# Kernel tuning notes

Measured on AMD Instinct MI355X. Metric: run time of the kernel, lower is better.

The kernel has to match this reference:

```python
import jax, jax.numpy as jnp
import numpy as np

N_NODES = 50000
N_EDGES = 800000
D_IN = 128
D_HID = 128
N_CLS = 40


def setup_inputs() -> dict:
    key = jax.random.key(0)
    ks = jax.random.split(key, 9)
    x = jax.random.normal(ks[0], (N_NODES, D_IN), dtype=jnp.float32)
    edge_index = jax.random.randint(ks[1], (2, N_EDGES), 0, N_NODES, dtype=jnp.int64)
    def lin(k, fan_in, fan_out):
        bound = 1.0 / np.sqrt(fan_in)
        return jax.random.uniform(k, (fan_in, fan_out), jnp.float32, -bound, bound)
    params = {
        'w1_l': lin(ks[2], D_IN, D_HID), 'w1_r': lin(ks[3], D_IN, D_HID),
        'b1': jnp.zeros((D_HID,), jnp.float32),
        'w2_l': lin(ks[4], D_HID, D_HID), 'w2_r': lin(ks[5], D_HID, D_HID),
        'b2': jnp.zeros((D_HID,), jnp.float32),
        'w3_l': lin(ks[6], D_HID, N_CLS), 'w3_r': lin(ks[7], D_HID, N_CLS),
        'b3': jnp.zeros((N_CLS,), jnp.float32),
    }
    return {'x': x, 'edge_index': edge_index, **params}


def _sage_layer(x, src, dst, w_l, w_r, b):
    # mean-aggregate messages from src -> dst, then lin_l(agg) + lin_r(x) + b, relu
    msgs = x[src]                                             # [E, d] gather
    agg = jax.ops.segment_sum(msgs, dst, num_segments=x.shape[0])  # [N, d]
    deg = jax.ops.segment_sum(jnp.ones((src.shape[0],), x.dtype), dst,
                              num_segments=x.shape[0])        # [N]
    agg = agg / jnp.maximum(deg, 1.0)[:, None]
    out = agg @ w_l + x @ w_r + b
    return jax.nn.relu(out)  # dropout p=0.0 -> identity


def reference(x, edge_index, w1_l, w1_r, b1, w2_l, w2_r, b2, w3_l, w3_r, b3):
    src, dst = edge_index[0], edge_index[1]
    h = _sage_layer(x, src, dst, w1_l, w1_r, b1)
    h = _sage_layer(h, src, dst, w2_l, w2_r, b2)
    h = _sage_layer(h, src, dst, w3_l, w3_r, b3)
    return h
```

## Files before the change

kernel.cpp:

```cpp
#include <hip/hip_runtime.h>
#include <hip/hip_bf16.h>

#define NN 50000
#define NE 800000
#define DD 128
#define NCLS 40
#define NBK ((NN + 255) >> 8)
#define EPB 1024
#define PB ((NE + EPB - 1) / EPB)
#define CVB ((NN * DD / 4) / 256)
#define WB 384
#define SEMAX 5120

typedef _Float16 f16x8 __attribute__((ext_vector_type(8)));
typedef _Float16 f16x4 __attribute__((ext_vector_type(4)));
typedef float f32x4 __attribute__((ext_vector_type(4)));

__device__ __forceinline__ unsigned int pack2h(_Float16 a, _Float16 b) {
    union { _Float16 h[2]; unsigned int u; } c;
    c.h[0] = a; c.h[1] = b;
    return c.u;
}
__device__ __forceinline__ void unpack2h(unsigned int p, float& a, float& b) {
    union { unsigned int u; _Float16 h[2]; } c;
    c.u = p;
    a = (float)c.h[0]; b = (float)c.h[1];
}

__global__ void k_front(const int* __restrict__ ei, int* __restrict__ cellcnt,
                        int* __restrict__ celloff, unsigned int* __restrict__ pairs,
                        const float* __restrict__ x, unsigned short* __restrict__ xh,
                        const float* __restrict__ w1l, const float* __restrict__ w1r,
                        const float* __restrict__ w2l, const float* __restrict__ w2r,
                        const float* __restrict__ w3l, const float* __restrict__ w3r,
                        unsigned short* __restrict__ bt1h,
                        unsigned short* __restrict__ bt2h,
                        unsigned short* __restrict__ bt3h) {
    if (blockIdx.x >= PB + CVB) {
        int idx = blockIdx.x - (PB + CVB);
        int w = idx >> 1, half = idx & 1;
        int ks = w & 7, tmp = w >> 3;
        int nt = tmp & 7, layer = tmp >> 3;
        const int NT = (layer == 2) ? 3 : 8;
        const int NC = (layer == 2) ? NCLS : DD;
        if (nt >= NT) return;
        const float* wl = (layer == 0) ? w1l : (layer == 1) ? w2l : w3l;
        const float* wr = (layer == 0) ? w1r : (layer == 1) ? w2r : w3r;
        unsigned short* bh = (layer == 0) ? bt1h : (layer == 1) ? bt2h : bt3h;
        int t = threadIdx.x;
        int j = t & 7, lane = (t >> 3) + half * 32;
        int row = nt * 16 + (lane & 15);
        int k = ks * 32 + (lane >> 4) * 8 + j;
        float v = 0.f;
        if (row < NC)
            v = (k < 128) ? wl[(size_t)k * NC + row] : wr[(size_t)(k - 128) * NC + row];
        union { _Float16 f; unsigned short u; } ch;
        ch.f = (_Float16)v;
        bh[((size_t)(ks * NT + nt) * 64 + lane) * 8 + j] = ch.u;
        return;
    }
    if (blockIdx.x >= PB) {
        int i = (blockIdx.x - PB) * 256 + threadIdx.x;
        float4 v = ((const float4*)x)[i];
        f16x4 h;
        h[0] = (_Float16)v.x; h[1] = (_Float16)v.y;
        h[2] = (_Float16)v.z; h[3] = (_Float16)v.w;
        *(f16x4*)(xh + (size_t)i * 4) = h;
        return;
    }
    __shared__ int hist[NBK];
    __shared__ int s[256];
    __shared__ unsigned int sE[EPB];
    __shared__ int nz;
    const int t = threadIdx.x, blk = blockIdx.x;
    const int e0 = blk * EPB;
    if (t == 0) nz = 0;
    for (int i = t; i < NBK; i += 256) hist[i] = 0;
    __syncthreads();
    int any = 0;
    for (int i = t; i < EPB; i += 256)
        if (ei[2 * e0 + 2 * i + 1] != 0) any = 1;
    if (any) atomicOr(&nz, 1);
    __syncthreads();
    const int is64 = (nz == 0);
    unsigned int v[EPB / 256];
    int eb[EPB / 256], er[EPB / 256];
#pragma unroll
    for (int j = 0; j < EPB / 256; ++j) {
        int e = e0 + j * 256 + t;
        if (e < NE) {
            int sv, d;
            if (is64) { sv = ei[2 * e]; d = ei[2 * (NE + e)]; }
            else      { sv = ei[e];     d = ei[NE + e]; }
            v[j] = ((unsigned)sv << 16) | (unsigned)d;
            eb[j] = d >> 8;
            er[j] = atomicAdd(&hist[eb[j]], 1);
        } else {
            eb[j] = -1;
        }
    }
    __syncthreads();
    int hv = (t < NBK) ? hist[t] : 0;
    s[t] = hv;
    __syncthreads();
#pragma unroll
    for (int off = 1; off < 256; off <<= 1) {
        int u = (t >= off) ? s[t - off] : 0;
        __syncthreads();
        s[t] += u;
        __syncthreads();
    }
#pragma unroll
    for (int j = 0; j < EPB / 256; ++j)
        if (eb[j] >= 0) sE[s[eb[j]] - hist[eb[j]] + er[j]] = v[j];
    __syncthreads();
    ((uint4*)(pairs + (size_t)blk * EPB))[t] = ((const uint4*)sE)[t];
    for (int i = t; i < NBK; i += 256) {
        cellcnt[(size_t)i * PB + blk] = hist[i];
        celloff[(size_t)i * PB + blk] = s[i] - hist[i];
    }
}

__global__ void k_scan_ba(const int* __restrict__ cellcnt, int* __restrict__ bsum) {
    __shared__ int red[256];
    int b = blockIdx.x, t = threadIdx.x;
    int acc = 0;
    for (int i = t; i < PB; i += 256) acc += cellcnt[(size_t)b * PB + i];
    red[t] = acc;
    __syncthreads();
#pragma unroll
    for (int off = 128; off > 0; off >>= 1) {
        if (t < off) red[t] += red[t + off];
        __syncthreads();
    }
    if (t == 0) bsum[b] = red[0];
}

__global__ void k_fill2(const unsigned int* __restrict__ pairs,
                        const int* __restrict__ cellcnt,
                        const int* __restrict__ celloff,
                        const int* __restrict__ bsum,
                        int* __restrict__ row_ptr, int* __restrict__ srcs) {
    __shared__ unsigned int sE[SEMAX];
    __shared__ int hist[256];
    __shared__ int cur[256];
    __shared__ int sb[256];
    __shared__ int scnt;
    const int b = blockIdx.x, t = threadIdx.x;
    if (t < 256) {
        int v = (t < NBK) ? bsum[t] : 0;
        sb[t] = v;
    }
    if (t == 0) scnt = 0;
    if (t < 256) hist[t] = 0;
    __syncthreads();
#pragma unroll
    for (int off = 1; off < 256; off <<= 1) {
        int u = (t >= off && t < 256) ? sb[t - off] : 0;
        __syncthreads();
        if (t < 256) sb[t] += u;
        __syncthreads();
    }
    const int bbase = (b == 0) ? 0 : sb[b - 1];
    if (b == NBK - 1 && t == 0) row_ptr[NN] = sb[NBK - 1];
    for (int blk = t; blk < PB; blk += 512) {
        int cnt = cellcnt[(size_t)b * PB + blk];
        if (cnt) {
            int off = celloff[(size_t)b * PB + blk];
            int base = atomicAdd(&scnt, cnt);
            if (base + cnt <= SEMAX) {
                const unsigned int* pp = pairs + (size_t)blk * EPB + off;
                for (int j = 0; j < cnt; ++j) {
                    unsigned int v = pp[j];
                    sE[base + j] = v;
                    atomicAdd(&hist[v & 255u], 1);
                }
            }
        }
    }
    __syncthreads();
    int h = (t < 256) ? hist[t] : 0;
    if (t < 256) cur[t] = h;
    __syncthreads();
#pragma unroll
    for (int off = 1; off < 256; off <<= 1) {
        int u = (t >= off && t < 256) ? cur[t - off] : 0;
        __syncthreads();
        if (t < 256) cur[t] += u;
        __syncthreads();
    }
    if (t < 256) {
        int node = (b << 8) + t;
        int base = bbase + cur[t] - h;
        if (node < NN) row_ptr[node] = base;
        cur[t] = base;
    }
    __syncthreads();
    int total = min(scnt, SEMAX);
    for (int i = t; i < total; i += 512) {
        unsigned int v = sE[i];
        int pos = atomicAdd(&cur[v & 255u], 1);
        srcs[pos] = (int)(v >> 16);
    }
}

__global__ __launch_bounds__(256, 8)
void k_agg(const unsigned int* __restrict__ inh, const int* __restrict__ row_ptr,
           const int* __restrict__ srcs, unsigned int* __restrict__ oh) {
    int node = blockIdx.x * 4 + (threadIdx.x >> 6);
    if (node >= NN) return;
    int lane = threadIdx.x & 63;
    int b = row_ptr[node], e = row_ptr[node + 1];
    float a0 = 0.f, a1 = 0.f;
    int i = b;
    for (; i + 16 <= e; i += 16) {
        unsigned int p[16];
#pragma unroll
        for (int j = 0; j < 16; ++j)
            p[j] = inh[(size_t)srcs[i + j] * 64 + lane];
#pragma unroll
        for (int j = 0; j < 16; ++j) {
            float u0, u1;
            unpack2h(p[j], u0, u1);
            a0 += u0; a1 += u1;
        }
    }
    int rem = e - i;
    if (rem > 0) {
        int ce = e - 1;
        unsigned int p[16];
#pragma unroll
        for (int j = 0; j < 16; ++j) {
            int idx = i + j;
            if (idx > ce) idx = ce;
            p[j] = inh[(size_t)srcs[idx] * 64 + lane];
        }
#pragma unroll
        for (int j = 0; j < 16; ++j) {
            float u0, u1;
            unpack2h(p[j], u0, u1);
            if (j < rem) { a0 += u0; a1 += u1; }
        }
    }
    int deg = e - b;
    float inv = 1.0f / (float)(deg > 0 ? deg : 1);
    oh[(size_t)node * 64 + lane] = pack2h((_Float16)(a0 * inv), (_Float16)(a1 * inv));
}

template <int NT, int KPS, bool PACKOUT>
__launch_bounds__(256, 4)
__global__ void k_mfma(const unsigned short* __restrict__ A1h,
                       const unsigned short* __restrict__ A2h,
                       const unsigned short* __restrict__ Bthf,
                       const float* __restrict__ bias, float* __restrict__ outf,
                       unsigned short* __restrict__ outh, const int NC) {
    constexpr int STAGE_ELEMS = KPS * NT * 64 * 8;
    constexpr int STAGE_U4 = STAGE_ELEMS / 8;
    __shared__ unsigned short sBh[STAGE_ELEMS];

    const int tid = threadIdx.x;
    const int wave = tid >> 6, lane = tid & 63;
    const int quad = lane >> 4, mr = lane & 15;
    const int m0 = blockIdx.x * 64 + wave * 16;
    const int row = m0 + mr;
    const bool rok = row < NN;

    f32x4 acc[NT] = {};
    const f16x8 zero = {};

    auto aload = [&](int ks) -> f16x8 {
        const int ko = ((ks * 32) & 127) + quad * 8;
        const unsigned short* base = (ks < 4) ? A1h : A2h;
        return rok ? *(const f16x8*)(base + (size_t)row * 128 + ko) : zero;
    };

    f16x8 cah = aload(0), pah;

#pragma unroll
    for (int s = 0; s < 8 / KPS; ++s) {
        const uint4* gh = (const uint4*)(Bthf + (size_t)s * STAGE_ELEMS);
        uint4* lh = (uint4*)sBh;
        if (s) __syncthreads();
        for (int i = tid; i < STAGE_U4; i += 256) lh[i] = gh[i];
        __syncthreads();

#pragma unroll
        for (int kl = 0; kl < KPS; ++kl) {
            const int ks = s * KPS + kl;
            if (ks < 7) pah = aload(ks + 1);
#pragma unroll
            for (int n = 0; n < NT; ++n) {
                const int fo = ((kl * NT + n) * 64 + lane) * 8;
                f16x8 bh = *(const f16x8*)(sBh + fo);
                acc[n] = __builtin_amdgcn_mfma_f32_16x16x32_f16(cah, bh, acc[n], 0, 0, 0);
            }
            cah = pah;
        }
    }

#pragma unroll
    for (int n = 0; n < NT; ++n) {
        int col = n * 16 + mr;
        float bv = (col < NC) ? bias[col] : 0.f;
#pragma unroll
        for (int r = 0; r < 4; ++r) {
            int orow = m0 + quad * 4 + r;
            if (orow < NN && col < NC) {
                float v = acc[n][r] + bv;
                v = v > 0.f ? v : 0.f;
                if (PACKOUT) {
                    union { _Float16 f; unsigned short u; } ch;
                    ch.f = (_Float16)v;
                    outh[(size_t)orow * 128 + col] = ch.u;
                } else {
                    outf[(size_t)orow * NC + col] = v;
                }
            }
        }
    }
}

__global__ __launch_bounds__(256, 4)
void k_gemm3(const unsigned short* __restrict__ Ah,
             const unsigned short* __restrict__ Bthf,
             const float* __restrict__ bias,
             unsigned short* __restrict__ zh, float* __restrict__ yf) {
    __shared__ unsigned short sBh[8 * 3 * 64 * 8];
    const int tid = threadIdx.x;
    const int wave = tid >> 6, lane = tid & 63;
    const int quad = lane >> 4, mr = lane & 15;
    const int m0 = blockIdx.x * 64 + wave * 16;
    const int row = m0 + mr;
    const bool rok = row < NN;

    const uint4* gh = (const uint4*)Bthf;
    uint4* lh = (uint4*)sBh;
    for (int i = tid; i < (8 * 3 * 64 * 8) / 8; i += 256) lh[i] = gh[i];

    const f16x8 zero = {};
    f16x8 a[4];
#pragma unroll
    for (int j = 0; j < 4; ++j)
        a[j] = rok ? *(const f16x8*)(Ah + (size_t)row * 128 + j * 32 + quad * 8)
                   : zero;
    __syncthreads();

    f32x4 accl[3] = {}, accr[3] = {};
#pragma unroll
    for (int ks = 0; ks < 4; ++ks) {
#pragma unroll
        for (int n = 0; n < 3; ++n) {
            f16x8 bl = *(const f16x8*)(sBh + ((ks * 3 + n) * 64 + lane) * 8);
            accl[n] = __builtin_amdgcn_mfma_f32_16x16x32_f16(a[ks], bl, accl[n], 0, 0, 0);
            f16x8 br = *(const f16x8*)(sBh + (((ks + 4) * 3 + n) * 64 + lane) * 8);
            accr[n] = __builtin_amdgcn_mfma_f32_16x16x32_f16(a[ks], br, accr[n], 0, 0, 0);
        }
    }

#pragma unroll
    for (int n = 0; n < 3; ++n) {
        int col = n * 16 + mr;
        float bv = (col < NCLS) ? bias[col] : 0.f;
#pragma unroll
        for (int r = 0; r < 4; ++r) {
            int orow = m0 + quad * 4 + r;
            if (orow < NN) {
                union { _Float16 f; unsigned short u; } ch;
                ch.f = (_Float16)accl[n][r];
                zh[(size_t)orow * 64 + col] = ch.u;
                if (col < NCLS) yf[(size_t)orow * 40 + col] = accr[n][r] + bv;
            }
        }
    }
}

__global__ __launch_bounds__(256, 8)
void k_agg3(const unsigned int* __restrict__ zu,
            const int* __restrict__ row_ptr,
            const int* __restrict__ srcs,
            const float* __restrict__ yf, float* __restrict__ out) {
    const int tid = threadIdx.x;
    const int wave = tid >> 6, lane = tid & 63;
    const int half = lane >> 5, hl = lane & 31;
    const int node = blockIdx.x * 8 + wave * 2 + half;
    int b = row_ptr[node], e = row_ptr[node + 1];
    int deg = e - b;
    int od = __shfl_xor(deg, 32);
    int md = max(deg, od);
    int ce = (e > b) ? (e - 1) : b;
    float a0 = 0.f, a1 = 0.f;
    for (int base = 0; base < md; base += 16) {
        unsigned int p[16];
#pragma unroll
        for (int j = 0; j < 16; ++j) {
            int idx = b + base + j;
            if (idx > ce) idx = ce;
            p[j] = zu[(size_t)srcs[idx] * 32 + hl];
        }
#pragma unroll
        for (int j = 0; j < 16; ++j) {
            float u0, u1;
            unpack2h(p[j], u0, u1);
            if (base + j < deg) { a0 += u0; a1 += u1; }
        }
    }
    float inv = 1.0f / (float)(deg > 0 ? deg : 1);
    if (hl < 20) {
        float2 yv = ((const float2*)yf)[(size_t)node * 20 + hl];
        float2 o;
        o.x = fmaxf(a0 * inv + yv.x, 0.f);
        o.y = fmaxf(a1 * inv + yv.y, 0.f);
        ((float2*)out)[(size_t)node * 20 + hl] = o;
    }
}

extern "C" void kernel_launch(void* const* d_in, const int* in_sizes, int n_in,
                              void* d_out, int out_size, void* d_ws, size_t ws_size,
                              hipStream_t stream) {
    const float* x    = (const float*)d_in[0];
    const int*   ei   = (const int*)d_in[1];
    const float* w1_l = (const float*)d_in[2];
    const float* w1_r = (const float*)d_in[3];
    const float* b1   = (const float*)d_in[4];
    const float* w2_l = (const float*)d_in[5];
    const float* w2_r = (const float*)d_in[6];
    const float* b2   = (const float*)d_in[7];
    const float* w3_l = (const float*)d_in[8];
    const float* w3_r = (const float*)d_in[9];
    const float* b3   = (const float*)d_in[10];
    float* out = (float*)d_out;

    char* w = (char*)d_ws;
    size_t off = 0;
    auto alloc = [&](size_t bytes) -> void* {
        void* p = w + off;
        off += (bytes + 255) / 256 * 256;
        return p;
    };
    int* row_ptr = (int*)alloc((size_t)(NN + 1) * 4);
    int* srcs    = (int*)alloc((size_t)NE * 4);
    int* cellcnt = (int*)alloc((size_t)NBK * PB * 4);
    int* celloff = (int*)alloc((size_t)NBK * PB * 4);
    int* bsum    = (int*)alloc((size_t)NBK * 4);
    unsigned int* pairs = (unsigned int*)alloc((size_t)PB * EPB * 4);
    unsigned short* xh   = (unsigned short*)alloc((size_t)NN * DD * 2);
    unsigned short* aggh = (unsigned short*)alloc((size_t)NN * DD * 2);
    unsigned short* h1h  = (unsigned short*)alloc((size_t)NN * DD * 2);
    unsigned short* zh   = (unsigned short*)alloc((size_t)NN * 64 * 2);
    float*          yf   = (float*)alloc((size_t)NN * 40 * 4);
    unsigned short* bt1h = (unsigned short*)alloc((size_t)8 * 8 * 64 * 8 * 2);
    unsigned short* bt2h = (unsigned short*)alloc((size_t)8 * 8 * 64 * 8 * 2);
    unsigned short* bt3h = (unsigned short*)alloc((size_t)8 * 3 * 64 * 8 * 2);
    unsigned short* h2h = xh;
    (void)ws_size;

    k_front<<<PB + CVB + WB, 256, 0, stream>>>(ei, cellcnt, celloff, pairs, x, xh,
                                               w1_l, w1_r, w2_l, w2_r, w3_l, w3_r,
                                               bt1h, bt2h, bt3h);
    k_scan_ba<<<NBK, 256, 0, stream>>>(cellcnt, bsum);
    k_fill2<<<NBK, 512, 0, stream>>>(pairs, cellcnt, celloff, bsum, row_ptr, srcs);

    const int gmb = (NN + 63) / 64;
    const int gab = (NN + 3) / 4;
    k_agg<<<gab, 256, 0, stream>>>((const unsigned int*)xh, row_ptr, srcs,
                                   (unsigned int*)aggh);
    k_mfma<8, 4, true><<<gmb, 256, 0, stream>>>(aggh, xh, bt1h, b1,
                                                nullptr, h1h, DD);
    k_agg<<<gab, 256, 0, stream>>>((const unsigned int*)h1h, row_ptr, srcs,
                                   (unsigned int*)aggh);
    k_mfma<8, 4, true><<<gmb, 256, 0, stream>>>(aggh, h1h, bt2h, b2,
                                                nullptr, h2h, DD);
    k_gemm3<<<gmb, 256, 0, stream>>>(h2h, bt3h, b3, zh, yf);
    k_agg3<<<NN / 8, 256, 0, stream>>>((const unsigned int*)zh, row_ptr, srcs,
                                       yf, out);
}
```

Baseline: 232.7 us.

## Split feature tables into column planes and use 16-bit source indices

Node feature tables are stored as four 32-column fp16 planes (each N x 64 bytes) instead of row-major 256-byte rows. The aggregation kernel now processes one plane per block, with blocks grouped by node pair and interleaved across planes, so each plane's gather working set is smaller and more likely to stay in cache. Source indices are narrowed to unsigned short to halve index traffic. The GEMM loads and stores are rewritten for the plane layout. Each gathered row segment is now only 64 bytes, which is short for coalescing. The 16-bit index is only valid because the packed value from the fill step holds the source in its upper 16 bits, and 50000 fits in that range.

```diff
diff --git a/kernel.cpp b/kernel.cpp
--- a/kernel.cpp
+++ b/kernel.cpp
@@ -26,6 +26,7 @@
     c.u = p;
     a = (float)c.h[0]; b = (float)c.h[1];
 }
+
 
 __global__ void k_front(const int* __restrict__ ei, int* __restrict__ cellcnt,
                         int* __restrict__ celloff, unsigned int* __restrict__ pairs,
@@ -65,7 +66,11 @@
         f16x4 h;
         h[0] = (_Float16)v.x; h[1] = (_Float16)v.y;
         h[2] = (_Float16)v.z; h[3] = (_Float16)v.w;
-        *(f16x4*)(xh + (size_t)i * 4) = h;
+        int row = i >> 5;
+        int f = i & 31;
+        int plane = f >> 3;
+        int pc = (f & 7) * 4;
+        *(f16x4*)(xh + ((size_t)plane * NN + row) * 32 + pc) = h;
         return;
     }
     __shared__ int hist[NBK];
@@ -140,7 +145,7 @@
                         const int* __restrict__ cellcnt,
                         const int* __restrict__ celloff,
                         const int* __restrict__ bsum,
-                        int* __restrict__ row_ptr, int* __restrict__ srcs) {
+                        int* __restrict__ row_ptr, unsigned short* __restrict__ srcs) {
     __shared__ unsigned int sE[SEMAX];
     __shared__ int hist[256];
     __shared__ int cur[256];
@@ -200,51 +205,48 @@
     for (int i = t; i < total; i += 512) {
         unsigned int v = sE[i];
         int pos = atomicAdd(&cur[v & 255u], 1);
-        srcs[pos] = (int)(v >> 16);
+        srcs[pos] = (unsigned short)(v >> 16);
     }
 }
 
 __global__ __launch_bounds__(256, 8)
-void k_agg(const unsigned int* __restrict__ inh, const int* __restrict__ row_ptr,
-           const int* __restrict__ srcs, unsigned int* __restrict__ oh) {
-    int node = blockIdx.x * 4 + (threadIdx.x >> 6);
-    if (node >= NN) return;
-    int lane = threadIdx.x & 63;
-    int b = row_ptr[node], e = row_ptr[node + 1];
+void k_agg8(const unsigned int* __restrict__ inq, const int* __restrict__ row_ptr,
+            const unsigned short* __restrict__ srcs, unsigned int* __restrict__ oq) {
+    const int tid = threadIdx.x;
+    const int quarter = (blockIdx.x & 7) >> 1;
+    const int parity  = blockIdx.x & 1;
+    const int node = ((blockIdx.x >> 3) * 2 + parity) * 16 + (tid >> 4);
+    const int pc = tid & 15;
+    const unsigned int* tab = inq + (size_t)quarter * NN * 16;
+    const int vn = node < NN ? node : NN - 1;
+    int b = row_ptr[vn], e = row_ptr[vn + 1];
+    int deg = (node < NN) ? (e - b) : 0;
+    int m = deg;
+    m = max(m, __shfl_xor(m, 16));
+    m = max(m, __shfl_xor(m, 32));
     float a0 = 0.f, a1 = 0.f;
-    int i = b;
-    for (; i + 16 <= e; i += 16) {
+    for (int base = 0; base < m; base += 16) {
         unsigned int p[16];
 #pragma unroll
-        for (int j = 0; j < 16; ++j)
-            p[j] = inh[(size_t)srcs[i + j] * 64 + lane];
+        for (int j = 0; j < 16; ++j) {
+            int idx = b + base + j;
+            idx = idx < e ? idx : (e - 1);
+            idx = idx < 0 ? 0 : idx;
+            idx = min(idx, NE - 1);
+            p[j] = tab[(size_t)srcs[idx] * 16 + pc];
+        }
 #pragma unroll
         for (int j = 0; j < 16; ++j) {
             float u0, u1;
             unpack2h(p[j], u0, u1);
-            a0 += u0; a1 += u1;
-        }
-    }
-    int rem = e - i;
-    if (rem > 0) {
-        int ce = e - 1;
-        unsigned int p[16];
-#pragma unroll
-        for (int j = 0; j < 16; ++j) {
-            int idx = i + j;
-            if (idx > ce) idx = ce;
-            p[j] = inh[(size_t)srcs[idx] * 64 + lane];
-        }
-#pragma unroll
-        for (int j = 0; j < 16; ++j) {
-            float u0, u1;
-            unpack2h(p[j], u0, u1);
-            if (j < rem) { a0 += u0; a1 += u1; }
-        }
-    }
-    int deg = e - b;
-    float inv = 1.0f / (float)(deg > 0 ? deg : 1);
-    oh[(size_t)node * 64 + lane] = pack2h((_Float16)(a0 * inv), (_Float16)(a1 * inv));
+            if (base + j < deg) { a0 += u0; a1 += u1; }
+        }
+    }
+    if (node < NN) {
+        float inv = 1.0f / (float)(deg > 0 ? deg : 1);
+        oq[((size_t)quarter * NN + node) * 16 + pc] =
+            pack2h((_Float16)(a0 * inv), (_Float16)(a1 * inv));
+    }
 }
 
 template <int NT, int KPS, bool PACKOUT>
@@ -269,9 +271,10 @@
     const f16x8 zero = {};
 
     auto aload = [&](int ks) -> f16x8 {
-        const int ko = ((ks * 32) & 127) + quad * 8;
         const unsigned short* base = (ks < 4) ? A1h : A2h;
-        return rok ? *(const f16x8*)(base + (size_t)row * 128 + ko) : zero;
+        const int plane = ks & 3;
+        return rok ? *(const f16x8*)(base + ((size_t)plane * NN + row) * 32 + quad * 8)
+                   : zero;
     };
 
     f16x8 cah = aload(0), pah;
@@ -311,7 +314,8 @@
                 if (PACKOUT) {
                     union { _Float16 f; unsigned short u; } ch;
                     ch.f = (_Float16)v;
-                    outh[(size_t)orow * 128 + col] = ch.u;
+                    int pl = col >> 5, pcc = col & 31;
+                    outh[((size_t)pl * NN + orow) * 32 + pcc] = ch.u;
                 } else {
                     outf[(size_t)orow * NC + col] = v;
                 }
@@ -341,7 +345,7 @@
     f16x8 a[4];
 #pragma unroll
     for (int j = 0; j < 4; ++j)
-        a[j] = rok ? *(const f16x8*)(Ah + (size_t)row * 128 + j * 32 + quad * 8)
+        a[j] = rok ? *(const f16x8*)(Ah + ((size_t)j * NN + row) * 32 + quad * 8)
                    : zero;
     __syncthreads();
 
@@ -377,7 +381,7 @@
 __global__ __launch_bounds__(256, 8)
 void k_agg3(const unsigned int* __restrict__ zu,
             const int* __restrict__ row_ptr,
-            const int* __restrict__ srcs,
+            const unsigned short* __restrict__ srcs,
             const float* __restrict__ yf, float* __restrict__ out) {
     const int tid = threadIdx.x;
     const int wave = tid >> 6, lane = tid & 63;
@@ -387,14 +391,15 @@
     int deg = e - b;
     int od = __shfl_xor(deg, 32);
     int md = max(deg, od);
-    int ce = (e > b) ? (e - 1) : b;
     float a0 = 0.f, a1 = 0.f;
     for (int base = 0; base < md; base += 16) {
         unsigned int p[16];
 #pragma unroll
         for (int j = 0; j < 16; ++j) {
             int idx = b + base + j;
-            if (idx > ce) idx = ce;
+            idx = idx < e ? idx : (e - 1);
+            idx = idx < 0 ? 0 : idx;
+            idx = min(idx, NE - 1);
             p[j] = zu[(size_t)srcs[idx] * 32 + hl];
         }
 #pragma unroll
@@ -438,7 +443,7 @@
         return p;
     };
     int* row_ptr = (int*)alloc((size_t)(NN + 1) * 4);
-    int* srcs    = (int*)alloc((size_t)NE * 4);
+    unsigned short* srcs = (unsigned short*)alloc((size_t)NE * 2 + 64);
     int* cellcnt = (int*)alloc((size_t)NBK * PB * 4);
     int* celloff = (int*)alloc((size_t)NBK * PB * 4);
     int* bsum    = (int*)alloc((size_t)NBK * 4);
@@ -461,12 +466,12 @@
     k_fill2<<<NBK, 512, 0, stream>>>(pairs, cellcnt, celloff, bsum, row_ptr, srcs);
 
     const int gmb = (NN + 63) / 64;
-    const int gab = (NN + 3) / 4;
-    k_agg<<<gab, 256, 0, stream>>>((const unsigned int*)xh, row_ptr, srcs,
+    const int gq = 8 * ((NN + 31) / 32);
+    k_agg8<<<gq, 256, 0, stream>>>((const unsigned int*)xh, row_ptr, srcs,
                                    (unsigned int*)aggh);
     k_mfma<8, 4, true><<<gmb, 256, 0, stream>>>(aggh, xh, bt1h, b1,
                                                 nullptr, h1h, DD);
-    k_agg<<<gab, 256, 0, stream>>>((const unsigned int*)h1h, row_ptr, srcs,
+    k_agg8<<<gq, 256, 0, stream>>>((const unsigned int*)h1h, row_ptr, srcs,
                                    (unsigned int*)aggh);
     k_mfma<8, 4, true><<<gmb, 256, 0, stream>>>(aggh, h1h, bt2h, b2,
                                                 nullptr, h2h, DD);
```

Measured after the change: 244.7 us. +5.2%, slower.

## Use 16-bit edge sources, exact-size tail gathers, and edge-split layer-3 aggregation

Applied to the files above, without the earlier changes.

The CSR source array now stores 16-bit node ids instead of 32-bit, which halves index traffic in every aggregation pass. This relies on the node count fitting in 16 bits. The padded, clamped 16-wide tail gathers are replaced by a cascade of 8/4/2/1-row chunks, so no redundant loads are issued for the leftover edges. The final-layer aggregation now gives one node per wave, with the two half-waves taking alternate edges and combining through a cross-lane shuffle, instead of packing two nodes per wave and padding to the larger degree.

```diff
diff --git a/kernel.cpp b/kernel.cpp
--- a/kernel.cpp
+++ b/kernel.cpp
@@ -140,7 +140,7 @@
                         const int* __restrict__ cellcnt,
                         const int* __restrict__ celloff,
                         const int* __restrict__ bsum,
-                        int* __restrict__ row_ptr, int* __restrict__ srcs) {
+                        int* __restrict__ row_ptr, unsigned short* __restrict__ srcs) {
     __shared__ unsigned int sE[SEMAX];
     __shared__ int hist[256];
     __shared__ int cur[256];
@@ -200,48 +200,40 @@
     for (int i = t; i < total; i += 512) {
         unsigned int v = sE[i];
         int pos = atomicAdd(&cur[v & 255u], 1);
-        srcs[pos] = (int)(v >> 16);
+        srcs[pos] = (unsigned short)(v >> 16);
+    }
+}
+
+template <int J>
+__device__ __forceinline__ void acc_rows(const unsigned int* __restrict__ inh,
+                                         const unsigned short* __restrict__ srcs,
+                                         int i, int lane, float& a0, float& a1) {
+    unsigned int p[J];
+#pragma unroll
+    for (int j = 0; j < J; ++j)
+        p[j] = inh[(size_t)srcs[i + j] * 64 + lane];
+#pragma unroll
+    for (int j = 0; j < J; ++j) {
+        float u0, u1;
+        unpack2h(p[j], u0, u1);
+        a0 += u0; a1 += u1;
     }
 }
 
 __global__ __launch_bounds__(256, 8)
 void k_agg(const unsigned int* __restrict__ inh, const int* __restrict__ row_ptr,
-           const int* __restrict__ srcs, unsigned int* __restrict__ oh) {
+           const unsigned short* __restrict__ srcs, unsigned int* __restrict__ oh) {
     int node = blockIdx.x * 4 + (threadIdx.x >> 6);
     if (node >= NN) return;
     int lane = threadIdx.x & 63;
     int b = row_ptr[node], e = row_ptr[node + 1];
     float a0 = 0.f, a1 = 0.f;
     int i = b;
-    for (; i + 16 <= e; i += 16) {
-        unsigned int p[16];
-#pragma unroll
-        for (int j = 0; j < 16; ++j)
-            p[j] = inh[(size_t)srcs[i + j] * 64 + lane];
-#pragma unroll
-        for (int j = 0; j < 16; ++j) {
-            float u0, u1;
-            unpack2h(p[j], u0, u1);
-            a0 += u0; a1 += u1;
-        }
-    }
-    int rem = e - i;
-    if (rem > 0) {
-        int ce = e - 1;
-        unsigned int p[16];
-#pragma unroll
-        for (int j = 0; j < 16; ++j) {
-            int idx = i + j;
-            if (idx > ce) idx = ce;
-            p[j] = inh[(size_t)srcs[idx] * 64 + lane];
-        }
-#pragma unroll
-        for (int j = 0; j < 16; ++j) {
-            float u0, u1;
-            unpack2h(p[j], u0, u1);
-            if (j < rem) { a0 += u0; a1 += u1; }
-        }
-    }
+    while (i + 16 <= e) { acc_rows<16>(inh, srcs, i, lane, a0, a1); i += 16; }
+    if (i + 8 <= e) { acc_rows<8>(inh, srcs, i, lane, a0, a1); i += 8; }
+    if (i + 4 <= e) { acc_rows<4>(inh, srcs, i, lane, a0, a1); i += 4; }
+    if (i + 2 <= e) { acc_rows<2>(inh, srcs, i, lane, a0, a1); i += 2; }
+    if (i < e)      { acc_rows<1>(inh, srcs, i, lane, a0, a1); }
     int deg = e - b;
     float inv = 1.0f / (float)(deg > 0 ? deg : 1);
     oh[(size_t)node * 64 + lane] = pack2h((_Float16)(a0 * inv), (_Float16)(a1 * inv));
@@ -374,43 +366,56 @@
     }
 }
 
+template <int J>
+__device__ __forceinline__ void acc_z(const unsigned int* __restrict__ zu,
+                                      const unsigned short* __restrict__ srcs,
+                                      int i0, int c, float& a0, float& a1) {
+    unsigned int p[J];
+#pragma unroll
+    for (int j = 0; j < J; ++j)
+        p[j] = zu[(size_t)srcs[i0 + 2 * j] * 32 + c];
+#pragma unroll
+    for (int j = 0; j < J; ++j) {
+        float u0, u1;
+        unpack2h(p[j], u0, u1);
+        a0 += u0; a1 += u1;
+    }
+}
+
 __global__ __launch_bounds__(256, 8)
 void k_agg3(const unsigned int* __restrict__ zu,
             const int* __restrict__ row_ptr,
-            const int* __restrict__ srcs,
+            const unsigned short* __restrict__ srcs,
             const float* __restrict__ yf, float* __restrict__ out) {
-    const int tid = threadIdx.x;
-    const int wave = tid >> 6, lane = tid & 63;
-    const int half = lane >> 5, hl = lane & 31;
-    const int node = blockIdx.x * 8 + wave * 2 + half;
-    int b = row_ptr[node], e = row_ptr[node + 1];
-    int deg = e - b;
-    int od = __shfl_xor(deg, 32);
-    int md = max(deg, od);
-    int ce = (e > b) ? (e - 1) : b;
+    const int node = blockIdx.x * 4 + (threadIdx.x >> 6);
+    const int lane = threadIdx.x & 63;
+    const int eg = lane >> 5;
+    const int c = lane & 31;
+    const int b = row_ptr[node], e = row_ptr[node + 1];
+    const int deg = e - b;
+    const int np = deg >> 1;
     float a0 = 0.f, a1 = 0.f;
-    for (int base = 0; base < md; base += 16) {
-        unsigned int p[16];
-#pragma unroll
-        for (int j = 0; j < 16; ++j) {
-            int idx = b + base + j;
-            if (idx > ce) idx = ce;
-            p[j] = zu[(size_t)srcs[idx] * 32 + hl];
-        }
-#pragma unroll
-        for (int j = 0; j < 16; ++j) {
-            float u0, u1;
-            unpack2h(p[j], u0, u1);
-            if (base + j < deg) { a0 += u0; a1 += u1; }
-        }
-    }
-    float inv = 1.0f / (float)(deg > 0 ? deg : 1);
-    if (hl < 20) {
-        float2 yv = ((const float2*)yf)[(size_t)node * 20 + hl];
+    const int i0 = b + eg;
+    int t = 0;
+    while (t + 8 <= np) { acc_z<8>(zu, srcs, i0 + 2 * t, c, a0, a1); t += 8; }
+    if (t + 4 <= np) { acc_z<4>(zu, srcs, i0 + 2 * t, c, a0, a1); t += 4; }
+    if (t + 2 <= np) { acc_z<2>(zu, srcs, i0 + 2 * t, c, a0, a1); t += 2; }
+    if (t < np)      { acc_z<1>(zu, srcs, i0 + 2 * t, c, a0, a1); }
+    if (deg & 1) {
+        unsigned int p = zu[(size_t)srcs[e - 1] * 32 + c];
+        float u0, u1;
+        unpack2h(p, u0, u1);
+        if (eg == 0) { a0 += u0; a1 += u1; }
+    }
+    a0 += __shfl_xor(a0, 32);
+    a1 += __shfl_xor(a1, 32);
+    if (eg == 0 && c < 20) {
+        float inv = 1.0f / (float)(deg > 0 ? deg : 1);
+        float2 yv = ((const float2*)yf)[(size_t)node * 20 + c];
         float2 o;
         o.x = fmaxf(a0 * inv + yv.x, 0.f);
         o.y = fmaxf(a1 * inv + yv.y, 0.f);
-        ((float2*)out)[(size_t)node * 20 + hl] = o;
+        ((float2*)out)[(size_t)node * 20 + c] = o;
     }
 }
 
@@ -438,7 +443,7 @@
         return p;
     };
     int* row_ptr = (int*)alloc((size_t)(NN + 1) * 4);
-    int* srcs    = (int*)alloc((size_t)NE * 4);
+    unsigned short* srcs = (unsigned short*)alloc((size_t)NE * 2 + 64);
     int* cellcnt = (int*)alloc((size_t)NBK * PB * 4);
     int* celloff = (int*)alloc((size_t)NBK * PB * 4);
     int* bsum    = (int*)alloc((size_t)NBK * 4);
@@ -471,6 +476,6 @@
     k_mfma<8, 4, true><<<gmb, 256, 0, stream>>>(aggh, h1h, bt2h, b2,
                                                 nullptr, h2h, DD);
     k_gemm3<<<gmb, 256, 0, stream>>>(h2h, bt3h, b3, zh, yf);
-    k_agg3<<<NN / 8, 256, 0, stream>>>((const unsigned int*)zh, row_ptr, srcs,
+    k_agg3<<<NN / 4, 256, 0, stream>>>((const unsigned int*)zh, row_ptr, srcs,
                                        yf, out);
 }
```

New measurement: 236.4 us. Within noise of the previous version (+1.6%).
